# Performance work log

Hardware: AMD Instinct MI355X
Metric: run time of the kernel (lower is better)

## Reference

```python
import jax, jax.numpy as jnp
import numpy as np

N_FEAT = 128
F_HID = 128


def setup_inputs() -> dict:
    key = jax.random.key(0)
    ks = jax.random.split(key, 9)
    N, E = 100000, 1600000
    x = jax.random.normal(ks[0], (N, N_FEAT), dtype=jnp.float32)
    edge_index = jax.random.randint(ks[1], (2, E), 0, N, dtype=jnp.int64)
    def glorot(k, fan_in, fan_out):
        lim = np.sqrt(6.0 / (fan_in + fan_out)).astype(np.float32)
        return jax.random.uniform(k, (fan_in, fan_out), jnp.float32, -lim, lim)
    return {
        "x": x,
        "edge_index": edge_index,
        "W1": glorot(ks[2], N_FEAT, F_HID), "b1": jnp.zeros((F_HID,), jnp.float32),
        "W2": glorot(ks[3], F_HID, F_HID), "b2": jnp.zeros((F_HID,), jnp.float32),
        "W3": glorot(ks[4], F_HID, F_HID), "b3": jnp.zeros((F_HID,), jnp.float32),
    }


def _gcn_conv(x, W, b, row, col, inv_sqrt_deg, n):
    # GCNConv: x' = D^{-1/2} (A + I) D^{-1/2} (x @ W) + b  (self-loops already in row/col)
    h = x @ W                                   # [N, F]
    norm = inv_sqrt_deg[row] * inv_sqrt_deg[col]  # [E']
    msg = h[col] * norm[:, None]                # gather + scale, [E', F]
    out = jax.ops.segment_sum(msg, row, num_segments=n)  # scatter-add, [N, F]
    return out + b


def reference(x, edge_index, W1, b1, W2, b2, W3, b3):
    n = x.shape[0]
    loops = jnp.arange(n, dtype=edge_index.dtype)
    row = jnp.concatenate([edge_index[0], loops])
    col = jnp.concatenate([edge_index[1], loops])
    deg = jax.ops.segment_sum(jnp.ones_like(row, dtype=x.dtype), row, num_segments=n)
    inv_sqrt_deg = jnp.where(deg > 0, jax.lax.rsqrt(jnp.maximum(deg, 1.0)), 0.0)
    h = _gcn_conv(x, W1, b1, row, col, inv_sqrt_deg, n)
    h = jax.nn.relu(h)  # dropout is identity in eval mode
    h = _gcn_conv(h, W2, b2, row, col, inv_sqrt_deg, n)
    h = jax.nn.relu(h)
    h = _gcn_conv(h, W3, b3, row, col, inv_sqrt_deg, n)
    return h
```

## Files before the change

### kernel.cpp

```cpp
#include <hip/hip_runtime.h>
#include <hip/hip_bf16.h>

#define NFEAT 128
#define EPB   4096
#define RPB   256
#define NBU_PAD 512
#define BCAP  6144

typedef short bf16x8 __attribute__((ext_vector_type(8)));
typedef float f32x4  __attribute__((ext_vector_type(4)));

__global__ __launch_bounds__(256) void a1_hist(const int* __restrict__ rows, int E,
                                               int* __restrict__ countsT, int nbu) {
    __shared__ int h[NBU_PAD];
    int t = threadIdx.x;
    for (int i = t; i < NBU_PAD; i += 256) h[i] = 0;
    __syncthreads();
    int e0 = blockIdx.x * EPB;
    int ecnt = min(EPB, E - e0);
    for (int k = t; k < ecnt; k += 256) atomicAdd(&h[rows[e0 + k] >> 8], 1);
    __syncthreads();
    for (int j = t; j < nbu; j += 256) countsT[(size_t)blockIdx.x * nbu + j] = h[j];
}

__global__ void transpose_counts(const int* __restrict__ in, int* __restrict__ out,
                                 int nbk, int nbu) {
    int i = blockIdx.x * 256 + threadIdx.x;
    if (i < nbk * nbu) {
        int b = i / nbk, blk = i - b * nbk;
        out[i] = in[(size_t)blk * nbu + b];
    }
}

#define SCAN_B 1024
__global__ void scanA_kernel(const int* __restrict__ in, int K,
                             int* __restrict__ excl, int* __restrict__ bsums) {
    __shared__ int sm[SCAN_B];
    int t = threadIdx.x;
    int g = blockIdx.x * SCAN_B + t;
    int v = (g < K) ? in[g] : 0;
    sm[t] = v;
    __syncthreads();
    for (int off = 1; off < SCAN_B; off <<= 1) {
        int u = (t >= off) ? sm[t - off] : 0;
        __syncthreads();
        sm[t] += u;
        __syncthreads();
    }
    if (g < K) excl[g] = sm[t] - v;
    if (t == SCAN_B - 1) bsums[blockIdx.x] = sm[t];
}

__global__ void scanB_kernel(int* __restrict__ bsums, int nb) {
    __shared__ int s[256];
    int t = threadIdx.x;
    int v = (t < nb) ? bsums[t] : 0;
    s[t] = v;
    __syncthreads();
    for (int off = 1; off < 256; off <<= 1) {
        int u = (t >= off) ? s[t - off] : 0;
        __syncthreads();
        s[t] += u;
        __syncthreads();
    }
    if (t < nb) bsums[t] = s[t] - v;
}

__global__ void scanC_kernel(int* __restrict__ excl, const int* __restrict__ bsums, int K) {
    int g = blockIdx.x * 256 + threadIdx.x;
    if (g < K) excl[g] += bsums[g >> 10];
}

__global__ __launch_bounds__(256) void a2_scatter(const int* __restrict__ rows,
                                                  const int* __restrict__ colsIn, int E,
                                                  const int* __restrict__ scanArr,
                                                  int nbk, int nbu,
                                                  int* __restrict__ packed) {
    __shared__ int cnt[NBU_PAD], start[NBU_PAD], cur[NBU_PAD];
    __shared__ int sortedV[EPB];
    __shared__ unsigned short sortedB[EPB];
    __shared__ int p[256];
    int t = threadIdx.x, blk = blockIdx.x;
    for (int i = t; i < NBU_PAD; i += 256) cnt[i] = 0;
    __syncthreads();
    int e0 = blk * EPB;
    int ecnt = min(EPB, E - e0);
    int myr[16], myc[16];
#pragma unroll
    for (int k = 0; k < 16; ++k) {
        int idx = k * 256 + t;
        if (idx < ecnt) {
            myr[k] = rows[e0 + idx];
            myc[k] = colsIn[e0 + idx];
            atomicAdd(&cnt[myr[k] >> 8], 1);
        }
    }
    __syncthreads();
    int a0 = cnt[2 * t], a1 = cnt[2 * t + 1];
    p[t] = a0 + a1;
    __syncthreads();
    for (int off = 1; off < 256; off <<= 1) {
        int u = (t >= off) ? p[t - off] : 0;
        __syncthreads();
        p[t] += u;
        __syncthreads();
    }
    int ex = p[t] - (a0 + a1);
    start[2 * t] = ex;      start[2 * t + 1] = ex + a0;
    cur[2 * t] = ex;        cur[2 * t + 1] = ex + a0;
    __syncthreads();
#pragma unroll
    for (int k = 0; k < 16; ++k) {
        int idx = k * 256 + t;
        if (idx < ecnt) {
            int b = myr[k] >> 8;
            int pos = atomicAdd(&cur[b], 1);
            sortedV[pos] = ((myr[k] & 255) << 17) | myc[k];
            sortedB[pos] = (unsigned short)b;
        }
    }
    __syncthreads();
    for (int j = t; j < nbu; j += 256) cnt[j] = scanArr[(size_t)j * nbk + blk] - start[j];
    __syncthreads();
    for (int i = t; i < ecnt; i += 256) {
        int b = sortedB[i];
        packed[cnt[b] + i] = sortedV[i];
    }
}

__global__ __launch_bounds__(256) void b_sort(const int* __restrict__ packed,
                                              const int* __restrict__ scanArr,
                                              int nbk, int nbu, int N, int E,
                                              int* __restrict__ colSort,
                                              int* __restrict__ row_ptr,
                                              float* __restrict__ inv) {
    __shared__ int cnt[RPB], start[RPB], cur[RPB], s[RPB];
    __shared__ int sv[BCAP];
    int t = threadIdx.x, b = blockIdx.x;
    int base = scanArr[(size_t)b * nbk];
    int nxt = (b + 1 < nbu) ? scanArr[(size_t)(b + 1) * nbk] : E;
    int sz = nxt - base;
    cnt[t] = 0;
    __syncthreads();
    for (int i = t; i < sz; i += 256) atomicAdd(&cnt[(packed[base + i] >> 17) & 255], 1);
    __syncthreads();
    int c = cnt[t];
    s[t] = c;
    __syncthreads();
    for (int off = 1; off < 256; off <<= 1) {
        int u = (t >= off) ? s[t - off] : 0;
        __syncthreads();
        s[t] += u;
        __syncthreads();
    }
    start[t] = s[t] - c;
    cur[t] = s[t] - c;
    __syncthreads();
    for (int i = t; i < sz; i += 256) {
        int v = packed[base + i];
        int lr = (v >> 17) & 255;
        int pos = atomicAdd(&cur[lr], 1);
        if (pos < BCAP) sv[pos] = v & 0x1FFFF;
    }
    __syncthreads();
    for (int i = t; i < sz; i += 256) colSort[base + i] = sv[i];
    int r = b * RPB + t;
    if (r < N) {
        row_ptr[r] = base + start[t];
        inv[r] = rsqrtf((float)(c + 1));
    }
    if (b == 0 && t == 0) row_ptr[N] = E;
}

__device__ inline unsigned short f2bf(float x) {
    unsigned u = __float_as_uint(x);
    unsigned r = (u + 0x7FFFu + ((u >> 16) & 1u)) >> 16;
    return (unsigned short)r;
}

__device__ inline void split2(float x0, float x1, unsigned& hw, unsigned& lw) {
    unsigned u0 = __float_as_uint(x0), u1 = __float_as_uint(x1);
    hw = (u1 & 0xFFFF0000u) | (u0 >> 16);
    float l0 = x0 - __uint_as_float(u0 & 0xFFFF0000u);
    float l1 = x1 - __uint_as_float(u1 & 0xFFFF0000u);
    lw = (__float_as_uint(l1) & 0xFFFF0000u) | (__float_as_uint(l0) >> 16);
}

__global__ void wsplit3_kernel(const float* __restrict__ W1, const float* __restrict__ W2,
                               const float* __restrict__ W3,
                               unsigned short* __restrict__ WtH,
                               unsigned short* __restrict__ WtL) {
    int w = blockIdx.y;
    const float* W = (w == 0) ? W1 : (w == 1) ? W2 : W3;
    int i = blockIdx.x * 256 + threadIdx.x;
    int c = i >> 7, k = i & 127;
    float wv = W[k * NFEAT + c];
    unsigned u = __float_as_uint(wv);
    unsigned hib = u & 0xFFFF0000u;
    float lo = wv - __uint_as_float(hib);
    WtH[w * NFEAT * NFEAT + i] = (unsigned short)(u >> 16);
    WtL[w * NFEAT * NFEAT + i] = (unsigned short)(__float_as_uint(lo) >> 16);
}

__global__ __launch_bounds__(256) void gemm_mfma_f32(const float* __restrict__ X,
                                                     const unsigned short* __restrict__ Wt_hi,
                                                     const unsigned short* __restrict__ Wt_lo,
                                                     const float* __restrict__ inv,
                                                     unsigned short* __restrict__ Hn, int n) {
    int tid = threadIdx.x;
    int wave = tid >> 6, lane = tid & 63;
    int lrow = lane & 15, kgrp = lane >> 4;
    int wcol0 = wave * 32;
    int rowbase = blockIdx.x * 64;

    bf16x8 bh[2][4], bl[2][4];
#pragma unroll
    for (int ct = 0; ct < 2; ++ct) {
        int col = wcol0 + ct * 16 + lrow;
        const unsigned short* ph = Wt_hi + (size_t)col * NFEAT + kgrp * 8;
        const unsigned short* pl = Wt_lo + (size_t)col * NFEAT + kgrp * 8;
#pragma unroll
        for (int ks = 0; ks < 4; ++ks) {
            bh[ct][ks] = *(const bf16x8*)(ph + ks * 32);
            bl[ct][ks] = *(const bf16x8*)(pl + ks * 32);
        }
    }

    union U8 { bf16x8 v; unsigned w[4]; };

#pragma unroll
    for (int rt = 0; rt < 4; ++rt) {
        int arow = rowbase + rt * 16 + lrow;
        int rc = arow < n ? arow : n - 1;
        const float* px = X + (size_t)rc * NFEAT + kgrp * 8;

        bf16x8 ah[4], al[4];
#pragma unroll
        for (int ks = 0; ks < 4; ++ks) {
            float4 v0 = *(const float4*)(px + ks * 32);
            float4 v1 = *(const float4*)(px + ks * 32 + 4);
            U8 uh, ul;
            split2(v0.x, v0.y, uh.w[0], ul.w[0]);
            split2(v0.z, v0.w, uh.w[1], ul.w[1]);
            split2(v1.x, v1.y, uh.w[2], ul.w[2]);
            split2(v1.z, v1.w, uh.w[3], ul.w[3]);
            ah[ks] = uh.v;
            al[ks] = ul.v;
        }

        f32x4 acc[2] = {{0.f, 0.f, 0.f, 0.f}, {0.f, 0.f, 0.f, 0.f}};
#pragma unroll
        for (int ks = 0; ks < 4; ++ks) {
#pragma unroll
            for (int ct = 0; ct < 2; ++ct) {
                acc[ct] = __builtin_amdgcn_mfma_f32_16x16x32_bf16(ah[ks], bh[ct][ks], acc[ct], 0, 0, 0);
                acc[ct] = __builtin_amdgcn_mfma_f32_16x16x32_bf16(ah[ks], bl[ct][ks], acc[ct], 0, 0, 0);
                acc[ct] = __builtin_amdgcn_mfma_f32_16x16x32_bf16(al[ks], bh[ct][ks], acc[ct], 0, 0, 0);
            }
        }

#pragma unroll
        for (int m = 0; m < 4; ++m) {
            int orow = rowbase + rt * 16 + kgrp * 4 + m;
            if (orow < n) {
                float sc = inv[orow];
#pragma unroll
                for (int ct = 0; ct < 2; ++ct) {
                    int col = wcol0 + ct * 16 + lrow;
                    Hn[(size_t)orow * NFEAT + col] = f2bf(acc[ct][m] * sc);
                }
            }
        }
    }
}

__global__ __launch_bounds__(256) void gemm_mfma_bf16(const unsigned short* __restrict__ XH,
                                                      const unsigned short* __restrict__ XL,
                                                      const unsigned short* __restrict__ Wt_hi,
                                                      const unsigned short* __restrict__ Wt_lo,
                                                      const float* __restrict__ inv,
                                                      unsigned short* __restrict__ Hn, int n) {
    int tid = threadIdx.x;
    int wave = tid >> 6, lane = tid & 63;
    int lrow = lane & 15, kgrp = lane >> 4;
    int wcol0 = wave * 32;
    int rowbase = blockIdx.x * 64;

    bf16x8 bh[2][4], bl[2][4];
#pragma unroll
    for (int ct = 0; ct < 2; ++ct) {
        int col = wcol0 + ct * 16 + lrow;
        const unsigned short* ph = Wt_hi + (size_t)col * NFEAT + kgrp * 8;
        const unsigned short* pl = Wt_lo + (size_t)col * NFEAT + kgrp * 8;
#pragma unroll
        for (int ks = 0; ks < 4; ++ks) {
            bh[ct][ks] = *(const bf16x8*)(ph + ks * 32);
            bl[ct][ks] = *(const bf16x8*)(pl + ks * 32);
        }
    }

#pragma unroll
    for (int rt = 0; rt < 4; ++rt) {
        int arow = rowbase + rt * 16 + lrow;
        int rc = arow < n ? arow : n - 1;
        const unsigned short* pxh = XH + (size_t)rc * NFEAT + kgrp * 8;
        const unsigned short* pxl = XL + (size_t)rc * NFEAT + kgrp * 8;

        bf16x8 ah[4], al[4];
#pragma unroll
        for (int ks = 0; ks < 4; ++ks) {
            ah[ks] = *(const bf16x8*)(pxh + ks * 32);
            al[ks] = *(const bf16x8*)(pxl + ks * 32);
        }

        f32x4 acc[2] = {{0.f, 0.f, 0.f, 0.f}, {0.f, 0.f, 0.f, 0.f}};
#pragma unroll
        for (int ks = 0; ks < 4; ++ks) {
#pragma unroll
            for (int ct = 0; ct < 2; ++ct) {
                acc[ct] = __builtin_amdgcn_mfma_f32_16x16x32_bf16(ah[ks], bh[ct][ks], acc[ct], 0, 0, 0);
                acc[ct] = __builtin_amdgcn_mfma_f32_16x16x32_bf16(ah[ks], bl[ct][ks], acc[ct], 0, 0, 0);
                acc[ct] = __builtin_amdgcn_mfma_f32_16x16x32_bf16(al[ks], bh[ct][ks], acc[ct], 0, 0, 0);
            }
        }

#pragma unroll
        for (int m = 0; m < 4; ++m) {
            int orow = rowbase + rt * 16 + kgrp * 4 + m;
            if (orow < n) {
                float sc = inv[orow];
#pragma unroll
                for (int ct = 0; ct < 2; ++ct) {
                    int col = wcol0 + ct * 16 + lrow;
                    Hn[(size_t)orow * NFEAT + col] = f2bf(acc[ct][m] * sc);
                }
            }
        }
    }
}

template <int RELU, int EMIT_SPLIT>
__global__ __launch_bounds__(256) void aggregate_bf16(const unsigned short* __restrict__ Hn,
                                                      const int* __restrict__ row_ptr,
                                                      const int* __restrict__ cols,
                                                      const float* __restrict__ inv,
                                                      const float* __restrict__ bias,
                                                      float* __restrict__ out,
                                                      unsigned short* __restrict__ XH,
                                                      unsigned short* __restrict__ XL, int n) {
    int node = blockIdx.x * (blockDim.x >> 6) + (threadIdx.x >> 6);
    if (node >= n) return;
    int lane = threadIdx.x & 63;
    int q = lane >> 4;
    int f = (lane & 15) << 3;

    float acc[8], acc2[8];
#pragma unroll
    for (int k = 0; k < 8; ++k) { acc[k] = 0.f; acc2[k] = 0.f; }

    if (q == 0) {
        uint4 v = *(const uint4*)(Hn + (size_t)node * NFEAT + f);
        const unsigned* u = (const unsigned*)&v;
#pragma unroll
        for (int k = 0; k < 4; ++k) {
            acc[2 * k]     = __uint_as_float(u[k] << 16);
            acc[2 * k + 1] = __uint_as_float(u[k] & 0xFFFF0000u);
        }
    }

    int s = row_ptr[node], e = row_ptr[node + 1];
    int j = s + q;
    for (; j + 4 < e; j += 8) {
        int ca = cols[j];
        int cb = cols[j + 4];
        uint4 va = *(const uint4*)(Hn + (size_t)ca * NFEAT + f);
        uint4 vb = *(const uint4*)(Hn + (size_t)cb * NFEAT + f);
        const unsigned* ua = (const unsigned*)&va;
        const unsigned* ub = (const unsigned*)&vb;
#pragma unroll
        for (int k = 0; k < 4; ++k) {
            acc[2 * k]      += __uint_as_float(ua[k] << 16);
            acc[2 * k + 1]  += __uint_as_float(ua[k] & 0xFFFF0000u);
            acc2[2 * k]     += __uint_as_float(ub[k] << 16);
            acc2[2 * k + 1] += __uint_as_float(ub[k] & 0xFFFF0000u);
        }
    }
    if (j < e) {
        int ca = cols[j];
        uint4 va = *(const uint4*)(Hn + (size_t)ca * NFEAT + f);
        const unsigned* ua = (const unsigned*)&va;
#pragma unroll
        for (int k = 0; k < 4; ++k) {
            acc[2 * k]     += __uint_as_float(ua[k] << 16);
            acc[2 * k + 1] += __uint_as_float(ua[k] & 0xFFFF0000u);
        }
    }
#pragma unroll
    for (int k = 0; k < 8; ++k) acc[k] += acc2[k];

#pragma unroll
    for (int k = 0; k < 8; ++k) {
        acc[k] += __shfl_xor(acc[k], 16, 64);
        acc[k] += __shfl_xor(acc[k], 32, 64);
    }

    if (q == 0) {
        float inv_i = inv[node];
        float4 b0 = *(const float4*)(bias + f);
        float4 b1v = *(const float4*)(bias + f + 4);
        float r[8];
        r[0] = acc[0] * inv_i + b0.x; r[1] = acc[1] * inv_i + b0.y;
        r[2] = acc[2] * inv_i + b0.z; r[3] = acc[3] * inv_i + b0.w;
        r[4] = acc[4] * inv_i + b1v.x; r[5] = acc[5] * inv_i + b1v.y;
        r[6] = acc[6] * inv_i + b1v.z; r[7] = acc[7] * inv_i + b1v.w;
        if (RELU) {
#pragma unroll
            for (int k = 0; k < 8; ++k) r[k] = fmaxf(r[k], 0.f);
        }
        if (EMIT_SPLIT) {
            ushort4 hv[2], lv[2];
#pragma unroll
            for (int g = 0; g < 2; ++g) {
#pragma unroll
                for (int k = 0; k < 4; ++k) {
                    float y = r[g * 4 + k];
                    unsigned u = __float_as_uint(y);
                    unsigned short hb = (unsigned short)(u >> 16);
                    float lo = y - __uint_as_float(u & 0xFFFF0000u);
                    ((unsigned short*)&hv[g])[k] = hb;
                    ((unsigned short*)&lv[g])[k] = f2bf(lo);
                }
            }
            *(ushort4*)(XH + (size_t)node * NFEAT + f)     = hv[0];
            *(ushort4*)(XH + (size_t)node * NFEAT + f + 4) = hv[1];
            *(ushort4*)(XL + (size_t)node * NFEAT + f)     = lv[0];
            *(ushort4*)(XL + (size_t)node * NFEAT + f + 4) = lv[1];
        } else {
            *(float4*)(out + (size_t)node * NFEAT + f)     = make_float4(r[0], r[1], r[2], r[3]);
            *(float4*)(out + (size_t)node * NFEAT + f + 4) = make_float4(r[4], r[5], r[6], r[7]);
        }
    }
}

static inline size_t align256(size_t x) { return (x + 255) & ~(size_t)255; }

extern "C" void kernel_launch(void* const* d_in, const int* in_sizes, int n_in,
                              void* d_out, int out_size, void* d_ws, size_t ws_size,
                              hipStream_t stream) {
    const float* x   = (const float*)d_in[0];
    const int*   ei  = (const int*)d_in[1];
    const float* W1  = (const float*)d_in[2];
    const float* b1  = (const float*)d_in[3];
    const float* W2  = (const float*)d_in[4];
    const float* b2  = (const float*)d_in[5];
    const float* W3  = (const float*)d_in[6];
    const float* b3  = (const float*)d_in[7];
    float* out = (float*)d_out;

    const int N = in_sizes[0] / NFEAT;
    const int E = in_sizes[1] / 2;
    const int* rows = ei;
    const int* colsIn = ei + E;

    const int nbk = (E + EPB - 1) / EPB;
    const int nbu = (N + RPB - 1) / RPB;
    const int K = nbk * nbu;

    char* ws = (char*)d_ws;
    size_t off = 0;
    unsigned short* Hn = (unsigned short*)(ws + off);
    off = align256(off + (size_t)N * NFEAT * sizeof(unsigned short));
    unsigned short* XH = (unsigned short*)(ws + off);
    off = align256(off + (size_t)N * NFEAT * sizeof(unsigned short));
    unsigned short* XL = (unsigned short*)(ws + off);
    off = align256(off + (size_t)N * NFEAT * sizeof(unsigned short));
    int*   bufA    = (int*)(ws + off);   off = align256(off + (size_t)K * sizeof(int));
    int*   bufB    = (int*)(ws + off);   off = align256(off + (size_t)K * sizeof(int));
    int*   bsums   = (int*)(ws + off);   off = align256(off + (size_t)256 * sizeof(int));
    int*   packed  = (int*)(ws + off);   off = align256(off + (size_t)E * sizeof(int));
    int*   colSort = (int*)(ws + off);   off = align256(off + (size_t)E * sizeof(int));
    int*   row_ptr = (int*)(ws + off);   off = align256(off + (size_t)(N + 1) * sizeof(int));
    float* inv     = (float*)(ws + off); off = align256(off + (size_t)N * sizeof(float));
    unsigned short* WtH = (unsigned short*)(ws + off);
    off = align256(off + (size_t)3 * NFEAT * NFEAT * sizeof(unsigned short));
    unsigned short* WtL = (unsigned short*)(ws + off);
    off = align256(off + (size_t)3 * NFEAT * NFEAT * sizeof(unsigned short));
    (void)ws_size; (void)n_in; (void)out_size;

    const int nb2 = (K + SCAN_B - 1) / SCAN_B;

    wsplit3_kernel<<<dim3(64, 3), 256, 0, stream>>>(W1, W2, W3, WtH, WtL);

    a1_hist<<<nbk, 256, 0, stream>>>(rows, E, bufA, nbu);
    transpose_counts<<<(K + 255) / 256, 256, 0, stream>>>(bufA, bufB, nbk, nbu);
    scanA_kernel<<<nb2, SCAN_B, 0, stream>>>(bufB, K, bufA, bsums);
    scanB_kernel<<<1, 256, 0, stream>>>(bsums, nb2);
    scanC_kernel<<<(K + 255) / 256, 256, 0, stream>>>(bufA, bsums, K);
    a2_scatter<<<nbk, 256, 0, stream>>>(rows, colsIn, E, bufA, nbk, nbu, packed);
    b_sort<<<nbu, 256, 0, stream>>>(packed, bufA, nbk, nbu, N, E, colSort, row_ptr, inv);

    const int gemm_grid = (N + 63) / 64;
    const int agg_grid  = (N + 3) / 4;

    gemm_mfma_f32<<<gemm_grid, 256, 0, stream>>>(x, WtH, WtL, inv, Hn, N);
    aggregate_bf16<1, 1><<<agg_grid, 256, 0, stream>>>(Hn, row_ptr, colSort, inv, b1,
                                                       nullptr, XH, XL, N);
    gemm_mfma_bf16<<<gemm_grid, 256, 0, stream>>>(XH, XL, WtH + NFEAT * NFEAT, WtL + NFEAT * NFEAT,
                                                  inv, Hn, N);
    aggregate_bf16<1, 1><<<agg_grid, 256, 0, stream>>>(Hn, row_ptr, colSort, inv, b2,
                                                       nullptr, XH, XL, N);
    gemm_mfma_bf16<<<gemm_grid, 256, 0, stream>>>(XH, XL, WtH + 2 * NFEAT * NFEAT,
                                                  WtL + 2 * NFEAT * NFEAT, inv, Hn, N);
    aggregate_bf16<0, 0><<<agg_grid, 256, 0, stream>>>(Hn, row_ptr, colSort, inv, b3,
                                                       out, nullptr, nullptr, N);
}
```

Before: 388.4 us.

## Fold scan block sums into consumers, prescale column offsets, unroll aggregation gather

```diff
diff --git a/kernel.cpp b/kernel.cpp
--- a/kernel.cpp
+++ b/kernel.cpp
@@ -66,14 +66,10 @@
     if (t < nb) bsums[t] = s[t] - v;
 }
 
-__global__ void scanC_kernel(int* __restrict__ excl, const int* __restrict__ bsums, int K) {
-    int g = blockIdx.x * 256 + threadIdx.x;
-    if (g < K) excl[g] += bsums[g >> 10];
-}
-
 __global__ __launch_bounds__(256) void a2_scatter(const int* __restrict__ rows,
                                                   const int* __restrict__ colsIn, int E,
                                                   const int* __restrict__ scanArr,
+                                                  const int* __restrict__ bsums,
                                                   int nbk, int nbu,
                                                   int* __restrict__ packed) {
     __shared__ int cnt[NBU_PAD], start[NBU_PAD], cur[NBU_PAD];
@@ -120,7 +116,10 @@
         }
     }
     __syncthreads();
-    for (int j = t; j < nbu; j += 256) cnt[j] = scanArr[(size_t)j * nbk + blk] - start[j];
+    for (int j = t; j < nbu; j += 256) {
+        int idx = j * nbk + blk;
+        cnt[j] = scanArr[idx] + bsums[idx >> 10] - start[j];
+    }
     __syncthreads();
     for (int i = t; i < ecnt; i += 256) {
         int b = sortedB[i];
@@ -130,6 +129,7 @@
 
 __global__ __launch_bounds__(256) void b_sort(const int* __restrict__ packed,
                                               const int* __restrict__ scanArr,
+                                              const int* __restrict__ bsums,
                                               int nbk, int nbu, int N, int E,
                                               int* __restrict__ colSort,
                                               int* __restrict__ row_ptr,
@@ -137,8 +137,13 @@
     __shared__ int cnt[RPB], start[RPB], cur[RPB], s[RPB];
     __shared__ int sv[BCAP];
     int t = threadIdx.x, b = blockIdx.x;
-    int base = scanArr[(size_t)b * nbk];
-    int nxt = (b + 1 < nbu) ? scanArr[(size_t)(b + 1) * nbk] : E;
+    int i0 = b * nbk;
+    int base = scanArr[i0] + bsums[i0 >> 10];
+    int nxt;
+    if (b + 1 < nbu) {
+        int i1 = (b + 1) * nbk;
+        nxt = scanArr[i1] + bsums[i1 >> 10];
+    } else nxt = E;
     int sz = nxt - base;
     cnt[t] = 0;
     __syncthreads();
@@ -163,7 +168,7 @@
         if (pos < BCAP) sv[pos] = v & 0x1FFFF;
     }
     __syncthreads();
-    for (int i = t; i < sz; i += 256) colSort[base + i] = sv[i];
+    for (int i = t; i < sz; i += 256) colSort[base + i] = sv[i] << 8;
     int r = b * RPB + t;
     if (r < N) {
         row_ptr[r] = base + start[t];
@@ -352,51 +357,81 @@
     if (node >= n) return;
     int lane = threadIdx.x & 63;
     int q = lane >> 4;
-    int f = (lane & 15) << 3;
-
-    float acc[8], acc2[8];
-#pragma unroll
-    for (int k = 0; k < 8; ++k) { acc[k] = 0.f; acc2[k] = 0.f; }
+    unsigned fb = (lane & 15) << 4;
+    const char* Hb = (const char*)Hn;
+
+    float2 accA[4], accB[4];
+#pragma unroll
+    for (int k = 0; k < 4; ++k) {
+        accA[k] = make_float2(0.f, 0.f);
+        accB[k] = make_float2(0.f, 0.f);
+    }
+
+#define UNPK_ADD(ACC, W) do {                                              \
+        unsigned _w = (W);                                                 \
+        float2 _t = make_float2(__uint_as_float(_w << 16),                 \
+                                __uint_as_float(_w & 0xFFFF0000u));        \
+        (ACC).x += _t.x; (ACC).y += _t.y;                                  \
+    } while (0)
 
     if (q == 0) {
-        uint4 v = *(const uint4*)(Hn + (size_t)node * NFEAT + f);
+        uint4 v = *(const uint4*)(Hb + ((unsigned)node << 8) + fb);
         const unsigned* u = (const unsigned*)&v;
 #pragma unroll
-        for (int k = 0; k < 4; ++k) {
-            acc[2 * k]     = __uint_as_float(u[k] << 16);
-            acc[2 * k + 1] = __uint_as_float(u[k] & 0xFFFF0000u);
-        }
+        for (int k = 0; k < 4; ++k) UNPK_ADD(accA[k], u[k]);
     }
 
     int s = row_ptr[node], e = row_ptr[node + 1];
     int j = s + q;
+    for (; j + 12 < e; j += 16) {
+        unsigned o0 = (unsigned)cols[j];
+        unsigned o1 = (unsigned)cols[j + 4];
+        unsigned o2 = (unsigned)cols[j + 8];
+        unsigned o3 = (unsigned)cols[j + 12];
+        uint4 v0 = *(const uint4*)(Hb + o0 + fb);
+        uint4 v1 = *(const uint4*)(Hb + o1 + fb);
+        uint4 v2 = *(const uint4*)(Hb + o2 + fb);
+        uint4 v3 = *(const uint4*)(Hb + o3 + fb);
+        const unsigned* u0 = (const unsigned*)&v0;
+        const unsigned* u1 = (const unsigned*)&v1;
+        const unsigned* u2 = (const unsigned*)&v2;
+        const unsigned* u3 = (const unsigned*)&v3;
+#pragma unroll
+        for (int k = 0; k < 4; ++k) {
+            UNPK_ADD(accA[k], u0[k]);
+            UNPK_ADD(accB[k], u1[k]);
+            UNPK_ADD(accA[k], u2[k]);
+            UNPK_ADD(accB[k], u3[k]);
+        }
+    }
     for (; j + 4 < e; j += 8) {
-        int ca = cols[j];
-        int cb = cols[j + 4];
-        uint4 va = *(const uint4*)(Hn + (size_t)ca * NFEAT + f);
-        uint4 vb = *(const uint4*)(Hn + (size_t)cb * NFEAT + f);
-        const unsigned* ua = (const unsigned*)&va;
-        const unsigned* ub = (const unsigned*)&vb;
+        unsigned o0 = (unsigned)cols[j];
+        unsigned o1 = (unsigned)cols[j + 4];
+        uint4 v0 = *(const uint4*)(Hb + o0 + fb);
+        uint4 v1 = *(const uint4*)(Hb + o1 + fb);
+        const unsigned* u0 = (const unsigned*)&v0;
+        const unsigned* u1 = (const unsigned*)&v1;
 #pragma unroll
         for (int k = 0; k < 4; ++k) {
-            acc[2 * k]      += __uint_as_float(ua[k] << 16);
-            acc[2 * k + 1]  += __uint_as_float(ua[k] & 0xFFFF0000u);
-            acc2[2 * k]     += __uint_as_float(ub[k] << 16);
-            acc2[2 * k + 1] += __uint_as_float(ub[k] & 0xFFFF0000u);
+            UNPK_ADD(accA[k], u0[k]);
+            UNPK_ADD(accB[k], u1[k]);
         }
     }
     if (j < e) {
-        int ca = cols[j];
-        uint4 va = *(const uint4*)(Hn + (size_t)ca * NFEAT + f);
-        const unsigned* ua = (const unsigned*)&va;
-#pragma unroll
-        for (int k = 0; k < 4; ++k) {
-            acc[2 * k]     += __uint_as_float(ua[k] << 16);
-            acc[2 * k + 1] += __uint_as_float(ua[k] & 0xFFFF0000u);
-        }
-    }
-#pragma unroll
-    for (int k = 0; k < 8; ++k) acc[k] += acc2[k];
+        unsigned o0 = (unsigned)cols[j];
+        uint4 v0 = *(const uint4*)(Hb + o0 + fb);
+        const unsigned* u0 = (const unsigned*)&v0;
+#pragma unroll
+        for (int k = 0; k < 4; ++k) UNPK_ADD(accA[k], u0[k]);
+    }
+#undef UNPK_ADD
+
+    float acc[8];
+#pragma unroll
+    for (int k = 0; k < 4; ++k) {
+        acc[2 * k]     = accA[k].x + accB[k].x;
+        acc[2 * k + 1] = accA[k].y + accB[k].y;
+    }
 
 #pragma unroll
     for (int k = 0; k < 8; ++k) {
@@ -405,6 +440,7 @@
     }
 
     if (q == 0) {
+        unsigned f = (lane & 15) << 3;
         float inv_i = inv[node];
         float4 b0 = *(const float4*)(bias + f);
         float4 b1v = *(const float4*)(bias + f + 4);
@@ -495,9 +531,8 @@
     transpose_counts<<<(K + 255) / 256, 256, 0, stream>>>(bufA, bufB, nbk, nbu);
     scanA_kernel<<<nb2, SCAN_B, 0, stream>>>(bufB, K, bufA, bsums);
     scanB_kernel<<<1, 256, 0, stream>>>(bsums, nb2);
-    scanC_kernel<<<(K + 255) / 256, 256, 0, stream>>>(bufA, bsums, K);
-    a2_scatter<<<nbk, 256, 0, stream>>>(rows, colsIn, E, bufA, nbk, nbu, packed);
-    b_sort<<<nbu, 256, 0, stream>>>(packed, bufA, nbk, nbu, N, E, colSort, row_ptr, inv);
+    a2_scatter<<<nbk, 256, 0, stream>>>(rows, colsIn, E, bufA, bsums, nbk, nbu, packed);
+    b_sort<<<nbu, 256, 0, stream>>>(packed, bufA, bsums, nbk, nbu, N, E, colSort, row_ptr, inv);
 
     const int gemm_grid = (N + 63) / 64;
     const int agg_grid  = (N + 3) / 4;
```

Measured after the change: 383.3 us. Within noise of the previous version (-1.3%).
